# Optimization experiments

Measured on AMD Instinct MI355X. Metric: run time of the kernel, lower is better.

The kernel has to match this reference:

```python
import jax, jax.numpy as jnp
import numpy as np

EPS = 1e-4          # self.epsilon
STENCIL = 24        # fixed neighbor count


def _apply_G(x, coeffs, neighbors, N):
    """SpMV: y_i = G_ii * x_i + sum_j G_ij * x_{nbr[i,j]}.
    x: [B,N,1], coeffs: [B,N,25], neighbors: [B,N,24] (>=N means invalid)."""
    B = x.shape[0]
    mask = neighbors < N                                   # [B,N,24]
    safe = jnp.where(mask, neighbors, 0)
    x2 = x[..., 0]                                         # [B,N]
    x_nbrs = jnp.take_along_axis(x2, safe.reshape(B, -1), axis=1)
    x_nbrs = x_nbrs.reshape(B, -1, STENCIL) * mask.astype(x.dtype)
    res = x2 * coeffs[:, :, 0] + (x_nbrs * coeffs[:, :, 1:]).sum(axis=2)
    return res[..., None]                                  # [B,N,1]


def _apply_GT(x, coeffs, neighbors, N):
    """Transpose SpMV (scatter-add): y_{nbr[i,j]} += G_ij * x_i."""
    B = x.shape[0]
    mask = neighbors < N
    tgt = jnp.where(mask, neighbors, 0)                    # safe targets; masked vals are 0
    vals = (x * coeffs[:, :, 1:]) * mask.astype(x.dtype)   # [B,N,24]
    res = x[..., 0] * coeffs[:, :, 0]                      # [B,N]
    res = jax.vmap(lambda r, t, v: r.at[t].add(v))(
        res, tgt.reshape(B, -1), vals.reshape(B, -1))
    return res[..., None]                                  # [B,N,1]


def setup_inputs() -> dict:
    key = jax.random.key(0)
    kG, kAd, kAo, kw, kn = jax.random.split(key, 5)
    B, N = 2, 262144
    G_coeffs = jax.random.normal(kG, (B, N, 25), dtype=jnp.float32)
    A_diag = jax.random.normal(kAd, (B, N, 1), dtype=jnp.float32)
    A_off = jax.random.normal(kAo, (B, N, STENCIL), dtype=jnp.float32)
    w = jax.random.normal(kw, (B, N, 1), dtype=jnp.float32)
    valid_mask = jnp.ones((B, N, 1), dtype=jnp.float32)
    neighbors = jax.random.randint(kn, (B, N, STENCIL), 0, 270000, dtype=jnp.int64)
    return {"G_coeffs": G_coeffs, "A_diag": A_diag, "A_off": A_off,
            "w": w, "valid_mask": valid_mask, "neighbors": neighbors}


def reference(G_coeffs, A_diag, A_off, w, valid_mask, neighbors):
    B, N, _ = G_coeffs.shape
    active = valid_mask.sum()
    norm_A = (jnp.abs(A_diag).sum() + jnp.abs(A_off).sum()) / (active * 25 + 1e-6)
    # single probe vector (num_probe_vectors = 1)
    wm = w * valid_mask                                    # probe, masked
    u = _apply_GT(wm, G_coeffs, neighbors, N)
    v = _apply_G(u, G_coeffs, neighbors, N) + EPS * wm
    A_coeffs = jnp.concatenate([A_diag, A_off], axis=2)    # [B,N,25]
    y = _apply_G(v, A_coeffs, neighbors, N)
    z = y / (norm_A + 1e-8)
    diff = (z - wm) * valid_mask
    return (diff ** 2).sum() / (valid_mask.sum() + 1e-6)
```

## Files before the change

kernel.cpp:

```cpp
#include <hip/hip_runtime.h>
#include <stdint.h>

#define STENCIL 24
#define EPS_F 1e-4f
#define BLK 256
#define NXCD 8

#define NODE_N 262144
#define BIN_NODES 2048
#define LBINS 128
#define NBINS 256
#define BIN_CAP_G 49152

#define S_THREADS 512
#define S_EPT 16
#define EDGES_PER_BLOCK (S_THREADS * S_EPT)

static __device__ __forceinline__ int get_xcc_id() {
    int x;
    asm volatile("s_getreg_b32 %0, hwreg(HW_REG_XCC_ID)" : "=s"(x));
    return x & (NXCD - 1);
}

__device__ __forceinline__ float wave_reduce_f32(float v) {
    #pragma unroll
    for (int off = 32; off > 0; off >>= 1)
        v += __shfl_down(v, off, 64);
    return v;
}

__device__ __forceinline__ float block_reduce_f32(float v) {
    __shared__ float sw[BLK / 64];
    float s = wave_reduce_f32(v);
    if ((threadIdx.x & 63) == 0) sw[threadIdx.x >> 6] = s;
    __syncthreads();
    float r = 0.f;
    if (threadIdx.x == 0) {
        #pragma unroll
        for (int k = 0; k < BLK / 64; ++k) r += sw[k];
    }
    return r;
}

__global__ void k_reduce(const float* __restrict__ Ad, const float* __restrict__ Ao,
                         const float* __restrict__ mask, long long BN,
                         float* __restrict__ pn, float* __restrict__ pa) {
    long long total = BN * STENCIL;
    long long stride = (long long)gridDim.x * blockDim.x;
    float s = 0.f, act = 0.f;
    for (long long t = (long long)blockIdx.x * blockDim.x + threadIdx.x; t < total; t += stride) {
        s += fabsf(Ao[t]);
        if (t < BN) { s += fabsf(Ad[t]); act += mask[t]; }
    }
    float bs = block_reduce_f32(s);
    if (threadIdx.x == 0) pn[blockIdx.x] = bs;
    __syncthreads();
    float ba = block_reduce_f32(act);
    if (threadIdx.x == 0) pa[blockIdx.x] = ba;
}

__global__ void k_scal(const float* __restrict__ pn, const float* __restrict__ pa,
                       int nblk, double* __restrict__ scal) {
    float sn = 0.f, sa = 0.f;
    for (int t = threadIdx.x; t < nblk; t += blockDim.x) { sn += pn[t]; sa += pa[t]; }
    float bn_ = block_reduce_f32(sn);
    __shared__ double dn;
    if (threadIdx.x == 0) dn = (double)bn_;
    __syncthreads();
    float ba = block_reduce_f32(sa);
    if (threadIdx.x == 0) {
        double act = (double)ba;
        scal[0] = dn / (act * 25.0 + 1e-6);
        scal[1] = act;
    }
}

__global__ __launch_bounds__(S_THREADS)
void k_sortscatter(const float* __restrict__ G, const float* __restrict__ w,
                   const float* __restrict__ mask, const int* __restrict__ nbr,
                   float* __restrict__ u, int* __restrict__ binCnt,
                   int2* __restrict__ pairs) {
    __shared__ int2 rec[EDGES_PER_BLOCK];
    __shared__ int hist[LBINS], incl[LBINS], excl[LBINS], pos[LBINS], gb[LBINS];
    int tid = threadIdx.x;
    if (tid < LBINS) hist[tid] = 0;
    __syncthreads();

    long long blockStart = (long long)blockIdx.x * EDGES_PER_BLOCK;
    long long t0 = blockStart + (long long)tid * S_EPT;

    int nb[S_EPT];
    const int4* p4 = (const int4*)(nbr + t0);
    #pragma unroll
    for (int q = 0; q < S_EPT / 4; ++q) {
        int4 x = p4[q];
        nb[q*4] = x.x; nb[q*4+1] = x.y; nb[q*4+2] = x.z; nb[q*4+3] = x.w;
    }
    #pragma unroll
    for (int e = 0; e < S_EPT; ++e) {
        unsigned n = (unsigned)nb[e];
        if (n < (unsigned)NODE_N) atomicAdd(&hist[n >> 11], 1);
    }
    __syncthreads();

    if (tid < LBINS) incl[tid] = hist[tid];
    __syncthreads();
    for (int d = 1; d < LBINS; d <<= 1) {
        int x = 0;
        if (tid < LBINS && tid >= d) x = incl[tid - d];
        __syncthreads();
        if (tid < LBINS) incl[tid] += x;
        __syncthreads();
    }
    int batchBase = (blockStart >= (long long)NODE_N * STENCIL) ? LBINS : 0;
    if (tid < LBINS) {
        int h = hist[tid];
        int ex = incl[tid] - h;
        excl[tid] = ex;
        pos[tid]  = ex;
        gb[tid]   = h ? atomicAdd(&binCnt[batchBase + tid], h) : 0;
    }
    __syncthreads();

    long long i0 = t0 / STENCIL;
    long long i1 = (t0 + S_EPT - 1) / STENCIL;
    float wm0 = w[i0] * mask[i0];
    float wm1 = (i1 != i0) ? w[i1] * mask[i1] : wm0;
    long long i = i0;
    int j = (int)(t0 - i0 * STENCIL);
    #pragma unroll
    for (int e = 0; e < S_EPT; ++e) {
        float wm = (i == i0) ? wm0 : wm1;
        if (j == 0) u[i] = wm * G[i * 25];
        unsigned n = (unsigned)nb[e];
        if (n < (unsigned)NODE_N) {
            int b = (int)(n >> 11);
            float val = wm * G[i * 25 + 1 + j];
            int lp = atomicAdd(&pos[b], 1);
            rec[lp] = make_int2((int)(n & (BIN_NODES - 1)) | (b << 11), __float_as_int(val));
        }
        if (++j == STENCIL) { j = 0; ++i; }
    }
    __syncthreads();

    int tot = incl[LBINS - 1];
    for (int s = tid; s < tot; s += S_THREADS) {
        int2 r = rec[s];
        int b = (r.x >> 11) & (LBINS - 1);
        int dst = gb[b] + (s - excl[b]);
        if (dst < BIN_CAP_G)
            pairs[(long long)(batchBase + b) * BIN_CAP_G + dst] =
                make_int2(r.x & (BIN_NODES - 1), r.y);
    }
}

__global__ __launch_bounds__(1024)
void k_binaccum(const int* __restrict__ binCnt, const int2* __restrict__ pairs,
                float* __restrict__ u) {
    __shared__ float acc[BIN_NODES];
    int g = blockIdx.x, tid = threadIdx.x;
    for (int l = tid; l < BIN_NODES; l += 1024) acc[l] = 0.f;
    __syncthreads();
    int cnt = binCnt[g]; if (cnt > BIN_CAP_G) cnt = BIN_CAP_G;
    const int2* pb = pairs + (long long)g * BIN_CAP_G;
    for (int s = tid; s < cnt; s += 1024) {
        int2 r = pb[s];
        atomicAdd(&acc[r.x], __int_as_float(r.y));
    }
    __syncthreads();
    long long gbase = (long long)(g >> 7) * NODE_N + (long long)(g & (LBINS - 1)) * BIN_NODES;
    for (int l = tid; l < BIN_NODES; l += 1024)
        u[gbase + l] += acc[l];
}

__global__ __launch_bounds__(BLK)
void k_v(const float* __restrict__ G, const float* __restrict__ w,
         const float* __restrict__ mask, const int* __restrict__ nbr,
         const float* __restrict__ u, float* __restrict__ v, long long BN) {
    __shared__ float sg[BLK * 25];
    int tid = threadIdx.x;
    long long blockBase = (long long)blockIdx.x * BLK;
    int rows = (int)((BN - blockBase) < BLK ? (BN - blockBase) : BLK);
    const float* gsrc = G + blockBase * 25;
    for (int k = tid; k < rows * 25; k += BLK) sg[k] = gsrc[k];
    __syncthreads();
    long long i = blockBase + tid;
    if (i >= BN) return;
    const float* g = sg + tid * 25;
    const int4* nb4 = (const int4*)(nbr + i * STENCIL);
    int nn[24];
    #pragma unroll
    for (int q = 0; q < 6; ++q) {
        int4 x = nb4[q];
        nn[q*4] = x.x; nn[q*4+1] = x.y; nn[q*4+2] = x.z; nn[q*4+3] = x.w;
    }
    const float* ub = u + (i / NODE_N) * (long long)NODE_N;
    float acc = u[i] * g[0] + EPS_F * w[i] * mask[i];
    #pragma unroll
    for (int jj = 0; jj < 24; ++jj) {
        int n = nn[jj];
        if ((unsigned)n < (unsigned)NODE_N) acc += g[1 + jj] * ub[n];
    }
    v[i] = acc;
}

__global__ __launch_bounds__(BLK)
void k_y(const float* __restrict__ Ad, const float* __restrict__ Ao,
         const float* __restrict__ w, const float* __restrict__ mask,
         const int* __restrict__ nbr, const float* __restrict__ v,
         const double* __restrict__ scal, float* __restrict__ py, long long BN) {
    long long i = (long long)blockIdx.x * BLK + threadIdx.x;
    float dsq = 0.f;
    if (i < BN) {
        const float4* ao4 = (const float4*)(Ao + i * STENCIL);
        const int4*   nb4 = (const int4*)(nbr + i * STENCIL);
        const float*  vb  = v + (i / NODE_N) * (long long)NODE_N;
        float acc = v[i] * Ad[i];
        #pragma unroll
        for (int q = 0; q < 6; ++q) {
            int4 x = nb4[q]; float4 a = ao4[q];
            if ((unsigned)x.x < (unsigned)NODE_N) acc += a.x * vb[x.x];
            if ((unsigned)x.y < (unsigned)NODE_N) acc += a.y * vb[x.y];
            if ((unsigned)x.z < (unsigned)NODE_N) acc += a.z * vb[x.z];
            if ((unsigned)x.w < (unsigned)NODE_N) acc += a.w * vb[x.w];
        }
        float z = acc / (float)(scal[0] + 1e-8);
        float m = mask[i];
        float d = (z - w[i] * m) * m;
        dsq = d * d;
    }
    float bs = block_reduce_f32(dsq);
    if (threadIdx.x == 0) py[blockIdx.x] = bs;
}

__global__ void k_final(const float* __restrict__ py, int nblk,
                        const double* __restrict__ scal, float* __restrict__ out) {
    float s = 0.f;
    for (int t = threadIdx.x; t < nblk; t += blockDim.x) s += py[t];
    float bs = block_reduce_f32(s);
    if (threadIdx.x == 0) out[0] = (float)((double)bs / (scal[1] + 1e-6));
}

__global__ void k_init_fb(const float* __restrict__ G, const float* __restrict__ w,
                          const float* __restrict__ mask, float* __restrict__ u, long long BN) {
    long long i = (long long)blockIdx.x * blockDim.x + threadIdx.x;
    if (i < BN) u[i] = w[i] * mask[i] * G[i * 25];
}
__global__ void k_scatter_fb(const float* __restrict__ G, const float* __restrict__ w,
                             const float* __restrict__ mask, const int* __restrict__ nbr,
                             float* __restrict__ ucopy, int N, long long BN) {
    long long t = (long long)blockIdx.x * blockDim.x + threadIdx.x;
    if (t >= BN * STENCIL) return;
    long long i = t / STENCIL;
    int j = (int)(t - i * STENCIL);
    int n = nbr[t];
    if ((unsigned)n >= (unsigned)N) return;
    float wm = w[i] * mask[i];
    float gv = G[i * 25 + 1 + j];
    float* ub = ucopy + (long long)get_xcc_id() * BN + (i / N) * (long long)N;
    __hip_atomic_fetch_add(&ub[n], wm * gv, __ATOMIC_RELAXED, __HIP_MEMORY_SCOPE_WORKGROUP);
}
__global__ void k_usum_fb(const float* __restrict__ ucopy, float* __restrict__ u, long long BN) {
    long long i = (long long)blockIdx.x * blockDim.x + threadIdx.x;
    if (i >= BN) return;
    float acc = u[i];
    #pragma unroll
    for (int c = 0; c < NXCD; ++c) acc += ucopy[(long long)c * BN + i];
    u[i] = acc;
}

extern "C" void kernel_launch(void* const* d_in, const int* in_sizes, int n_in,
                              void* d_out, int out_size, void* d_ws, size_t ws_size,
                              hipStream_t stream) {
    const float* G    = (const float*)d_in[0];
    const float* Ad   = (const float*)d_in[1];
    const float* Ao   = (const float*)d_in[2];
    const float* w    = (const float*)d_in[3];
    const float* mask = (const float*)d_in[4];
    const int*   nbr  = (const int*)d_in[5];

    const long long BN = in_sizes[3];
    const long long nEdges = BN * STENCIL;
    const int nodeBlocks = (int)((BN + BLK - 1) / BLK);

    float* u  = (float*)d_ws;
    float* v  = u + BN;
    float* pn = v + BN;
    float* pa = pn + 1024;
    float* py = pa + 1024;
    char*  after_common = (char*)(py + nodeBlocks);

    int*  binCnt = (int*)(((uintptr_t)after_common + 15) & ~(uintptr_t)15);
    int2* pairs  = (int2*)(((uintptr_t)(binCnt + NBINS) + 7) & ~(uintptr_t)7);
    double* scal_fast = (double*)(((uintptr_t)(pairs + (long long)NBINS * BIN_CAP_G) + 7) & ~(uintptr_t)7);
    size_t need_fast = (size_t)((char*)(scal_fast + 2) - (char*)d_ws);

    float* ucopy = (float*)(((uintptr_t)after_common + 15) & ~(uintptr_t)15);
    double* scal_fb = (double*)(((uintptr_t)(ucopy + (long long)NXCD * BN) + 7) & ~(uintptr_t)7);

    bool fast = (BN == 2LL * NODE_N) && (ws_size >= need_fast);

    k_reduce<<<1024, BLK, 0, stream>>>(Ad, Ao, mask, BN, pn, pa);

    if (fast) {
        double* scal = scal_fast;
        k_scal<<<1, BLK, 0, stream>>>(pn, pa, 1024, scal);
        hipMemsetAsync(binCnt, 0, NBINS * sizeof(int), stream);
        int gridS = (int)(nEdges / EDGES_PER_BLOCK);
        k_sortscatter<<<gridS, S_THREADS, 0, stream>>>(G, w, mask, nbr, u, binCnt, pairs);
        k_binaccum<<<NBINS, 1024, 0, stream>>>(binCnt, pairs, u);
        k_v<<<(int)(BN / BLK), BLK, 0, stream>>>(G, w, mask, nbr, u, v, BN);
        k_y<<<nodeBlocks, BLK, 0, stream>>>(Ad, Ao, w, mask, nbr, v, scal, py, BN);
        k_final<<<1, BLK, 0, stream>>>(py, nodeBlocks, scal, (float*)d_out);
    } else {
        double* scal = scal_fb;
        k_scal<<<1, BLK, 0, stream>>>(pn, pa, 1024, scal);
        hipMemsetAsync(ucopy, 0, (size_t)NXCD * BN * sizeof(float), stream);
        int edgeBlocks = (int)((nEdges + BLK - 1) / BLK);
        k_init_fb<<<nodeBlocks, BLK, 0, stream>>>(G, w, mask, u, BN);
        k_scatter_fb<<<edgeBlocks, BLK, 0, stream>>>(G, w, mask, nbr, ucopy, NODE_N, BN);
        k_usum_fb<<<nodeBlocks, BLK, 0, stream>>>(ucopy, u, BN);
        k_v<<<nodeBlocks, BLK, 0, stream>>>(G, w, mask, nbr, u, v, BN);
        k_y<<<nodeBlocks, BLK, 0, stream>>>(Ad, Ao, w, mask, nbr, v, scal, py, BN);
        k_final<<<1, BLK, 0, stream>>>(py, nodeBlocks, scal, (float*)d_out);
    }
}
```

Measured before the change: 474.3 us.

## Coalesce streaming loads via shared-memory staging and nontemporal hints

Switches streaming reads of coefficients, neighbors, w and mask to nontemporal loads so they do not evict the gathered vectors u and v from cache. The sort-scatter kernel now reads edges in a thread-strided pattern, so each wave's loads are coalesced, and it computes edge values during the first pass. The k_v and k_y kernels stage per-row neighbor indices and coefficients into LDS with coalesced loads, padded to a 25-element row stride, instead of per-thread vector loads. This costs more LDS per block, which may lower occupancy, and adds integer division in the staging loops.

New measurement: 531.2 us. 1.12x slower.

```diff
diff --git a/kernel.cpp b/kernel.cpp
--- a/kernel.cpp
+++ b/kernel.cpp
@@ -15,6 +15,13 @@
 #define S_THREADS 512
 #define S_EPT 16
 #define EDGES_PER_BLOCK (S_THREADS * S_EPT)
+
+typedef int   i32x2 __attribute__((ext_vector_type(2)));
+
+template <typename T>
+static __device__ __forceinline__ T ntload(const T* p) {
+    return __builtin_nontemporal_load(p);
+}
 
 static __device__ __forceinline__ int get_xcc_id() {
     int x;
@@ -49,8 +56,8 @@
     long long stride = (long long)gridDim.x * blockDim.x;
     float s = 0.f, act = 0.f;
     for (long long t = (long long)blockIdx.x * blockDim.x + threadIdx.x; t < total; t += stride) {
-        s += fabsf(Ao[t]);
-        if (t < BN) { s += fabsf(Ad[t]); act += mask[t]; }
+        s += fabsf(ntload(Ao + t));
+        if (t < BN) { s += fabsf(ntload(Ad + t)); act += ntload(mask + t); }
     }
     float bs = block_reduce_f32(s);
     if (threadIdx.x == 0) pn[blockIdx.x] = bs;
@@ -87,19 +94,20 @@
     __syncthreads();
 
     long long blockStart = (long long)blockIdx.x * EDGES_PER_BLOCK;
-    long long t0 = blockStart + (long long)tid * S_EPT;
 
     int nb[S_EPT];
-    const int4* p4 = (const int4*)(nbr + t0);
-    #pragma unroll
-    for (int q = 0; q < S_EPT / 4; ++q) {
-        int4 x = p4[q];
-        nb[q*4] = x.x; nb[q*4+1] = x.y; nb[q*4+2] = x.z; nb[q*4+3] = x.w;
-    }
+    float val[S_EPT];
     #pragma unroll
     for (int e = 0; e < S_EPT; ++e) {
-        unsigned n = (unsigned)nb[e];
-        if (n < (unsigned)NODE_N) atomicAdd(&hist[n >> 11], 1);
+        long long t = blockStart + (long long)e * S_THREADS + tid;
+        long long i = t / STENCIL;
+        int j = (int)(t - i * STENCIL);
+        int n = ntload(nbr + t);
+        nb[e] = n;
+        float wm = ntload(w + i) * ntload(mask + i);
+        if (j == 0) u[i] = wm * ntload(G + i * 25);
+        val[e] = wm * ntload(G + i * 25 + 1 + j);
+        if ((unsigned)n < (unsigned)NODE_N) atomicAdd(&hist[n >> 11], 1);
     }
     __syncthreads();
 
@@ -122,24 +130,15 @@
     }
     __syncthreads();
 
-    long long i0 = t0 / STENCIL;
-    long long i1 = (t0 + S_EPT - 1) / STENCIL;
-    float wm0 = w[i0] * mask[i0];
-    float wm1 = (i1 != i0) ? w[i1] * mask[i1] : wm0;
-    long long i = i0;
-    int j = (int)(t0 - i0 * STENCIL);
     #pragma unroll
     for (int e = 0; e < S_EPT; ++e) {
-        float wm = (i == i0) ? wm0 : wm1;
-        if (j == 0) u[i] = wm * G[i * 25];
         unsigned n = (unsigned)nb[e];
         if (n < (unsigned)NODE_N) {
             int b = (int)(n >> 11);
-            float val = wm * G[i * 25 + 1 + j];
             int lp = atomicAdd(&pos[b], 1);
-            rec[lp] = make_int2((int)(n & (BIN_NODES - 1)) | (b << 11), __float_as_int(val));
+            rec[lp] = make_int2((int)(n & (BIN_NODES - 1)) | (b << 11),
+                                __float_as_int(val[e]));
         }
-        if (++j == STENCIL) { j = 0; ++i; }
     }
     __syncthreads();
 
@@ -162,9 +161,9 @@
     for (int l = tid; l < BIN_NODES; l += 1024) acc[l] = 0.f;
     __syncthreads();
     int cnt = binCnt[g]; if (cnt > BIN_CAP_G) cnt = BIN_CAP_G;
-    const int2* pb = pairs + (long long)g * BIN_CAP_G;
+    const i32x2* pb = (const i32x2*)(pairs + (long long)g * BIN_CAP_G);
     for (int s = tid; s < cnt; s += 1024) {
-        int2 r = pb[s];
+        i32x2 r = __builtin_nontemporal_load(pb + s);
         atomicAdd(&acc[r.x], __int_as_float(r.y));
     }
     __syncthreads();
@@ -178,28 +177,28 @@
          const float* __restrict__ mask, const int* __restrict__ nbr,
          const float* __restrict__ u, float* __restrict__ v, long long BN) {
     __shared__ float sg[BLK * 25];
+    __shared__ int  snb[BLK * 25];
     int tid = threadIdx.x;
-    long long blockBase = (long long)blockIdx.x * BLK;
-    int rows = (int)((BN - blockBase) < BLK ? (BN - blockBase) : BLK);
-    const float* gsrc = G + blockBase * 25;
-    for (int k = tid; k < rows * 25; k += BLK) sg[k] = gsrc[k];
-    __syncthreads();
-    long long i = blockBase + tid;
-    if (i >= BN) return;
-    const float* g = sg + tid * 25;
-    const int4* nb4 = (const int4*)(nbr + i * STENCIL);
-    int nn[24];
-    #pragma unroll
-    for (int q = 0; q < 6; ++q) {
-        int4 x = nb4[q];
-        nn[q*4] = x.x; nn[q*4+1] = x.y; nn[q*4+2] = x.z; nn[q*4+3] = x.w;
-    }
+    long long base = (long long)blockIdx.x * BLK;
+    int rows = (int)(((BN - base) < BLK) ? (BN - base) : BLK);
+    const float* gsrc = G + base * 25;
+    for (int k = tid; k < rows * 25; k += BLK) sg[k] = ntload(gsrc + k);
+    const int* nsrc = nbr + base * STENCIL;
+    for (int k = tid; k < rows * STENCIL; k += BLK) {
+        int r = k / STENCIL, c = k - r * STENCIL;
+        snb[r * 25 + c] = ntload(nsrc + k);
+    }
+    __syncthreads();
+    if (tid >= rows) return;
+    long long i = base + tid;
+    const float* g  = sg + tid * 25;
+    const int*   nn = snb + tid * 25;
     const float* ub = u + (i / NODE_N) * (long long)NODE_N;
-    float acc = u[i] * g[0] + EPS_F * w[i] * mask[i];
-    #pragma unroll
-    for (int jj = 0; jj < 24; ++jj) {
-        int n = nn[jj];
-        if ((unsigned)n < (unsigned)NODE_N) acc += g[1 + jj] * ub[n];
+    float acc = u[i] * g[0] + EPS_F * ntload(w + i) * ntload(mask + i);
+    #pragma unroll
+    for (int j = 0; j < STENCIL; ++j) {
+        int n = nn[j];
+        if ((unsigned)n < (unsigned)NODE_N) acc += g[1 + j] * ub[n];
     }
     v[i] = acc;
 }
@@ -209,24 +208,34 @@
          const float* __restrict__ w, const float* __restrict__ mask,
          const int* __restrict__ nbr, const float* __restrict__ v,
          const double* __restrict__ scal, float* __restrict__ py, long long BN) {
-    long long i = (long long)blockIdx.x * BLK + threadIdx.x;
+    __shared__ float sa[BLK * 25];
+    __shared__ int  snb[BLK * 25];
+    int tid = threadIdx.x;
+    long long base = (long long)blockIdx.x * BLK;
+    int rows = (int)(((BN - base) < BLK) ? (BN - base) : BLK);
+    const float* asrc = Ao + base * STENCIL;
+    const int*   nsrc = nbr + base * STENCIL;
+    for (int k = tid; k < rows * STENCIL; k += BLK) {
+        int r = k / STENCIL, c = k - r * STENCIL;
+        sa[r * 25 + c]  = ntload(asrc + k);
+        snb[r * 25 + c] = ntload(nsrc + k);
+    }
+    __syncthreads();
     float dsq = 0.f;
-    if (i < BN) {
-        const float4* ao4 = (const float4*)(Ao + i * STENCIL);
-        const int4*   nb4 = (const int4*)(nbr + i * STENCIL);
-        const float*  vb  = v + (i / NODE_N) * (long long)NODE_N;
-        float acc = v[i] * Ad[i];
+    if (tid < rows) {
+        long long i = base + tid;
+        const float* a  = sa + tid * 25;
+        const int*   nn = snb + tid * 25;
+        const float* vb = v + (i / NODE_N) * (long long)NODE_N;
+        float acc = v[i] * ntload(Ad + i);
         #pragma unroll
-        for (int q = 0; q < 6; ++q) {
-            int4 x = nb4[q]; float4 a = ao4[q];
-            if ((unsigned)x.x < (unsigned)NODE_N) acc += a.x * vb[x.x];
-            if ((unsigned)x.y < (unsigned)NODE_N) acc += a.y * vb[x.y];
-            if ((unsigned)x.z < (unsigned)NODE_N) acc += a.z * vb[x.z];
-            if ((unsigned)x.w < (unsigned)NODE_N) acc += a.w * vb[x.w];
+        for (int j = 0; j < STENCIL; ++j) {
+            int n = nn[j];
+            if ((unsigned)n < (unsigned)NODE_N) acc += a[j] * vb[n];
         }
         float z = acc / (float)(scal[0] + 1e-8);
-        float m = mask[i];
-        float d = (z - w[i] * m) * m;
+        float m = ntload(mask + i);
+        float d = (z - ntload(w + i) * m) * m;
         dsq = d * d;
     }
     float bs = block_reduce_f32(dsq);
```
